# Performance work log

Hardware: AMD Instinct MI355X
Metric: run time of the kernel (lower is better)

The kernel has to match this reference:

```python
import jax, jax.numpy as jnp
import numpy as np

B, S, D, H, E, K = 2, 2048, 1024, 4096, 8, 2


def setup_inputs() -> dict:
    key = jax.random.key(0)
    ks = jax.random.split(key, 7)
    sd = 1.0 / np.sqrt(D)
    sh = 1.0 / np.sqrt(H)
    return {
        "x": jax.random.normal(ks[0], (B, S, D), dtype=jnp.float32),
        "Wr": jax.random.uniform(ks[1], (D, E), jnp.float32, -sd, sd),
        "br": jnp.zeros((E,), jnp.float32),
        "W1": jax.random.uniform(ks[2], (E, D, H), jnp.float32, -sd, sd),
        "b1": jax.random.uniform(ks[3], (E, H), jnp.float32, -sd, sd),
        "W2": jax.random.uniform(ks[4], (E, H, D), jnp.float32, -sh, sh),
        "b2": jax.random.uniform(ks[5], (E, D), jnp.float32, -sh, sh),
    }


def reference(x, Wr, br, W1, b1, W2, b2):
    # Router
    router_logits = jnp.einsum("bsd,de->bse", x, Wr) + br          # [B,S,E]
    topk_logits, topk_idx = jax.lax.top_k(router_logits, K)          # [B,S,K]
    gates = jax.nn.softmax(topk_logits, axis=-1)                     # [B,S,K]

    # Dense all-expert FFN (math identical to masked per-expert GEMMs)
    h = jax.nn.gelu(jnp.einsum("bsd,edh->ebsh", x, W1) + b1[:, None, None, :],
                    approximate=False)                                # [E,B,S,H]
    y = jnp.einsum("ebsh,ehd->bsed", h, W2) + b2[None, None, :, :]    # [B,S,E,D]

    # Gather the top-k experts per token and combine with gates
    sel = jnp.take_along_axis(y, topk_idx[..., None], axis=2)         # [B,S,K,D]
    out = jnp.sum(gates[..., None] * sel, axis=2)                     # [B,S,D]

    # Load-balancing aux loss
    probs = jax.nn.softmax(router_logits, axis=-1)
    importance = probs.mean(axis=(0, 1))                              # [E]
    aux_loss = jnp.mean((importance - 1.0 / E) ** 2)
    return out, aux_loss
```

## Files before the change

### kernel.cpp

```cpp
#include <hip/hip_runtime.h>
#include <hip/hip_bf16.h>
#include <math.h>

#define NTOK 4096
#define DD   1024
#define HH   4096
#define EE   8
#define NSLOT 8192
#define NSLOT_PAD 8320
#define RBLK 128

typedef __bf16 bf16x8 __attribute__((ext_vector_type(8)));
typedef float  f32x4  __attribute__((ext_vector_type(4)));
typedef unsigned short u16x8 __attribute__((ext_vector_type(8)));

#define WAITCNT_VM(n) (((n) & 0xF) | (0x7 << 4) | (0xF << 8) | (((n) >> 4) << 14))

#define WS_COUNTS     0
#define WS_CURSORS    64
#define WS_OFFSETS    128
#define WS_IMP        256
#define WS_TOPK_IDX   512
#define WS_TOPK_GATE  33280
#define WS_SLOT_OF    66048
#define WS_TOKEN_LIST 98816
#define WS_XG         131584
#define WS_HBUF       17170944
#define WS_YBUF       85328384
#define WS_W1BT       118882816
#define WS_W2BT       185991680
#define WS_CNT_PART   (WS_HBUF + (size_t)NSLOT * HH * 2)
#define WS_IMP_PART   (WS_HBUF + (size_t)NSLOT * HH * 2 + 4096)

__device__ __forceinline__ float gelu_exact(float v) {
    return 0.5f * v * (1.0f + erff(v * 0.70710678118654752f));
}

__device__ __forceinline__ void async_copy16(const __bf16* g, __bf16* l) {
    __builtin_amdgcn_global_load_lds(
        (const __attribute__((address_space(1))) void*)g,
        (__attribute__((address_space(3))) void*)l, 16, 0, 0);
}

__launch_bounds__(256)
__global__ void router_kernel(const float* __restrict__ x,
                              const float* __restrict__ Wr,
                              const float* __restrict__ br,
                              int* __restrict__ cntPart,
                              float* __restrict__ impPart,
                              int* __restrict__ topk_idx,
                              float* __restrict__ topk_gate) {
    __shared__ float WrL[DD * EE];
    __shared__ float impW[4][EE];
    __shared__ int cntL[EE];
    int tid = threadIdx.x;
    int lane = tid & 63, wave = tid >> 6;
    int grp = lane >> 3, e = lane & 7;
    int t = blockIdx.x * 32 + wave * 8 + grp;

    for (int i = tid; i < DD * EE / 4; i += 256)
        ((float4*)WrL)[i] = ((const float4*)Wr)[i];
    if (tid < EE) cntL[tid] = 0;
    __syncthreads();

    const float* xr = x + (size_t)t * DD;
    float acc = 0.f;
#pragma unroll 4
    for (int d = 0; d < DD; d += 4) {
        float4 xv = *(const float4*)(xr + d);
        acc = fmaf(xv.x, WrL[(d + 0) * EE + e], acc);
        acc = fmaf(xv.y, WrL[(d + 1) * EE + e], acc);
        acc = fmaf(xv.z, WrL[(d + 2) * EE + e], acc);
        acc = fmaf(xv.w, WrL[(d + 3) * EE + e], acc);
    }
    float l = acc + br[e];

    float m = l;
#pragma unroll
    for (int mk = 1; mk <= 4; mk <<= 1) m = fmaxf(m, __shfl_xor(m, mk, 64));
    float p = expf(l - m);
    float s = p;
#pragma unroll
    for (int mk = 1; mk <= 4; mk <<= 1) s += __shfl_xor(s, mk, 64);
    p /= s;

    float bl = l; int be = e;
#pragma unroll
    for (int mk = 1; mk <= 4; mk <<= 1) {
        float ol = __shfl_xor(bl, mk, 64);
        int   oe = __shfl_xor(be, mk, 64);
        if (ol > bl || (ol == bl && oe < be)) { bl = ol; be = oe; }
    }
    int e1 = be; float l1 = bl;
    float cl = (e == e1) ? -INFINITY : l; int ce = e;
#pragma unroll
    for (int mk = 1; mk <= 4; mk <<= 1) {
        float ol = __shfl_xor(cl, mk, 64);
        int   oe = __shfl_xor(ce, mk, 64);
        if (ol > cl || (ol == cl && oe < ce)) { cl = ol; ce = oe; }
    }
    int e2 = ce; float l2 = cl;

    if (e == 0) {
        float bb = expf(l2 - l1);
        float g1 = 1.f / (1.f + bb);
        topk_idx[t * 2 + 0] = e1; topk_idx[t * 2 + 1] = e2;
        topk_gate[t * 2 + 0] = g1; topk_gate[t * 2 + 1] = bb * g1;
        atomicAdd(&cntL[e1], 1);
        atomicAdd(&cntL[e2], 1);
    }

#pragma unroll
    for (int mk = 8; mk <= 32; mk <<= 1) p += __shfl_xor(p, mk, 64);
    if (lane < 8) impW[wave][lane] = p;
    __syncthreads();
    if (tid < EE) {
        float v = impW[0][tid] + impW[1][tid] + impW[2][tid] + impW[3][tid];
        impPart[blockIdx.x * EE + tid] = v;
        cntPart[blockIdx.x * EE + tid] = cntL[tid];
    }
}

__launch_bounds__(64)
__global__ void prefix_kernel(const int* __restrict__ cntPart,
                              const float* __restrict__ impPart,
                              int* __restrict__ offsets,
                              int* __restrict__ cursors,
                              float* __restrict__ aux_out) {
    __shared__ int cs[EE];
    __shared__ float is[EE];
    int tid = threadIdx.x;
    if (tid < EE) {
        int c = 0; float v = 0.f;
        for (int b = 0; b < RBLK; b++) {
            c += cntPart[b * EE + tid];
            v += impPart[b * EE + tid];
        }
        cs[tid] = c; is[tid] = v;
    }
    __syncthreads();
    if (tid == 0) {
        int o = 0;
        for (int e = 0; e < EE; e++) { offsets[e] = o; cursors[e] = o; o += cs[e]; }
        offsets[EE] = o;
        float aux = 0.f;
        for (int e = 0; e < EE; e++) {
            float d = is[e] / (float)NTOK - 1.0f / (float)EE;
            aux += d * d;
        }
        aux_out[0] = aux / (float)EE;
    }
}

__launch_bounds__(256)
__global__ void scatter_kernel(const int* __restrict__ topk_idx,
                               int* __restrict__ cursors,
                               int* __restrict__ token_list,
                               int* __restrict__ slot_of) {
    __shared__ int lcnt[EE];
    __shared__ int lbase[EE];
    int tid = threadIdx.x;
    int t = blockIdx.x * 256 + tid;
    if (tid < EE) lcnt[tid] = 0;
    __syncthreads();
    int e0 = topk_idx[t * 2 + 0], e1 = topk_idx[t * 2 + 1];
    int r0 = atomicAdd(&lcnt[e0], 1);
    int r1 = atomicAdd(&lcnt[e1], 1);
    __syncthreads();
    if (tid < EE) lbase[tid] = atomicAdd(&cursors[tid], lcnt[tid]);
    __syncthreads();
    int s0 = lbase[e0] + r0, s1 = lbase[e1] + r1;
    token_list[s0] = t; token_list[s1] = t;
    slot_of[t * 2 + 0] = s0; slot_of[t * 2 + 1] = s1;
}

__launch_bounds__(256)
__global__ void gather_x_kernel(const float* __restrict__ x,
                                const int* __restrict__ token_list,
                                __bf16* __restrict__ xg) {
    int s = blockIdx.x;
    int t = token_list[s];
    int tid = threadIdx.x;
    float4 v = ((const float4*)(x + (size_t)t * DD))[tid];
    __bf16 tmp[4] __attribute__((aligned(8)));
    tmp[0] = (__bf16)v.x; tmp[1] = (__bf16)v.y;
    tmp[2] = (__bf16)v.z; tmp[3] = (__bf16)v.w;
    ((ushort4*)(xg + (size_t)s * DD))[tid] = *(ushort4*)tmp;
}

__launch_bounds__(256)
__global__ void transpose_w_kernel(const float* __restrict__ in,
                                   __bf16* __restrict__ out,
                                   int R, int C) {
    int e = blockIdx.z;
    int c0 = blockIdx.x * 64, r0 = blockIdx.y * 64;
    __shared__ float tile[64][65];
    int tid = threadIdx.x;
    const float* ip = in + (size_t)e * R * C;
#pragma unroll
    for (int i = 0; i < 4; i++) {
        int flat = i * 256 + tid;
        int r = flat >> 4, c4 = (flat & 15) * 4;
        float4 v = *(const float4*)(ip + (size_t)(r0 + r) * C + c0 + c4);
        tile[r][c4 + 0] = v.x; tile[r][c4 + 1] = v.y;
        tile[r][c4 + 2] = v.z; tile[r][c4 + 3] = v.w;
    }
    __syncthreads();
    __bf16* op = out + (size_t)e * C * R;
#pragma unroll
    for (int i = 0; i < 2; i++) {
        int flat = i * 256 + tid;
        int c = flat >> 3, r8 = (flat & 7) * 8;
        __bf16 tmp[8] __attribute__((aligned(16)));
#pragma unroll
        for (int j = 0; j < 8; j++) tmp[j] = (__bf16)tile[r8 + j][c];
        *(u16x8*)(op + (size_t)(c0 + c) * R + r0 + r8) = *(u16x8*)tmp;
    }
}

template <int N, int K, bool GELU, typename OutT>
__launch_bounds__(256, 2)
__global__ void gemm_bt_kernel(const __bf16* __restrict__ A,
                               const __bf16* __restrict__ Bt,
                               const float* __restrict__ bias,
                               const int* __restrict__ offsets,
                               OutT* __restrict__ Out) {
    int e = blockIdx.z, ct = blockIdx.x, rt = blockIdx.y;
    int obase = offsets[e], cnt = offsets[e + 1] - obase;
    int m0 = rt * 128;
    if (m0 >= cnt) return;

    __shared__ __bf16 As[2][128 * 64];
    __shared__ __bf16 Bs[2][128 * 64];

    int tid = threadIdx.x, lane = tid & 63, wave = tid >> 6;
    int quad = lane >> 4, m16 = lane & 15;
    int wm = wave & 1, wn = wave >> 1;
    int srow = lane >> 3;
    int scol = ((lane & 7) ^ srow) * 8;
    int swz = m16 & 7;

    const __bf16* Ag = A + (size_t)(obase + m0) * K;
    const __bf16* Bg = Bt + ((size_t)e * N + (size_t)ct * 128) * K;

    f32x4 acc[4][4] = {};

#define STAGE(buf, k0)                                                        \
    {                                                                         \
        _Pragma("unroll")                                                     \
        for (int r = 0; r < 4; r++) {                                         \
            int chunk = r * 4 + wave;                       \
            int row = chunk * 8 + srow;                                       \
            async_copy16(Ag + (size_t)row * K + (k0) + scol, As[buf] + chunk * 512); \
        }                                                                     \
        _Pragma("unroll")                                                     \
        for (int r = 0; r < 4; r++) {                                         \
            int chunk = r * 4 + wave;                                         \
            int row = chunk * 8 + srow;                                       \
            async_copy16(Bg + (size_t)row * K + (k0) + scol, Bs[buf] + chunk * 512); \
        }                                                                     \
    }

#define COMPUTE(buf)                                                          \
    {                                                                         \
        const __bf16* Ac = As[buf];                                           \
        const __bf16* Bc = Bs[buf];                                           \
        _Pragma("unroll")                                                     \
        for (int kk = 0; kk < 64; kk += 32) {                                 \
            int kkc = kk >> 3;                                                \
            bf16x8 af[4], bfr[4];                                             \
            _Pragma("unroll")                                                 \
            for (int mi = 0; mi < 4; mi++)                                    \
                af[mi] = *(const bf16x8*)(Ac + (wm * 64 + mi * 16 + m16) * 64 \
                                          + (((kkc + quad) ^ swz) * 8));      \
            _Pragma("unroll")                                                 \
            for (int ni = 0; ni < 4; ni++)                                    \
                bfr[ni] = *(const bf16x8*)(Bc + (wn * 64 + ni * 16 + m16) * 64\
                                           + (((kkc + quad) ^ swz) * 8));     \
            _Pragma("unroll")                                                 \
            for (int mi = 0; mi < 4; mi++)                                    \
                _Pragma("unroll")                                             \
                for (int ni = 0; ni < 4; ni++)                                \
                    acc[mi][ni] = __builtin_amdgcn_mfma_f32_16x16x32_bf16(    \
                        af[mi], bfr[ni], acc[mi][ni], 0, 0, 0);               \
        }                                                                     \
    }

    STAGE(0, 0);
    int cur = 0;
    for (int k0 = 64; k0 < K; k0 += 64) {
        STAGE(cur ^ 1, k0);
        __builtin_amdgcn_s_waitcnt(WAITCNT_VM(8));
        __builtin_amdgcn_s_barrier();
        COMPUTE(cur);
        __builtin_amdgcn_s_barrier();
        cur ^= 1;
    }
    __builtin_amdgcn_s_waitcnt(WAITCNT_VM(0));
    __builtin_amdgcn_s_barrier();
    COMPUTE(cur);
#undef STAGE
#undef COMPUTE

    float bv[4];
#pragma unroll
    for (int ni = 0; ni < 4; ni++)
        bv[ni] = bias[(size_t)e * N + ct * 128 + wn * 64 + ni * 16 + m16];
#pragma unroll
    for (int mi = 0; mi < 4; mi++) {
#pragma unroll
        for (int r = 0; r < 4; r++) {
            int row = wm * 64 + mi * 16 + quad * 4 + r;
            if (m0 + row < cnt) {
                size_t orow = (size_t)(obase + m0 + row) * N + (size_t)ct * 128 + wn * 64;
#pragma unroll
                for (int ni = 0; ni < 4; ni++) {
                    float v = acc[mi][ni][r] + bv[ni];
                    if (GELU) v = gelu_exact(v);
                    Out[orow + ni * 16 + m16] = (OutT)v;
                }
            }
        }
    }
}

__launch_bounds__(256)
__global__ void combine_kernel(const float* __restrict__ ybuf,
                               const int* __restrict__ slot_of,
                               const float* __restrict__ topk_gate,
                               float* __restrict__ out) {
    int t = blockIdx.x;
    int tid = threadIdx.x;
    int s0 = slot_of[t * 2 + 0], s1 = slot_of[t * 2 + 1];
    float g0 = topk_gate[t * 2 + 0], g1 = topk_gate[t * 2 + 1];
    const float4* y0 = (const float4*)(ybuf + (size_t)s0 * DD);
    const float4* y1 = (const float4*)(ybuf + (size_t)s1 * DD);
    float4 a = y0[tid], b = y1[tid];
    float4 o;
    o.x = g0 * a.x + g1 * b.x;
    o.y = g0 * a.y + g1 * b.y;
    o.z = g0 * a.z + g1 * b.z;
    o.w = g0 * a.w + g1 * b.w;
    ((float4*)(out + (size_t)t * DD))[tid] = o;
}

extern "C" void kernel_launch(void* const* d_in, const int* in_sizes, int n_in,
                              void* d_out, int out_size, void* d_ws, size_t ws_size,
                              hipStream_t stream) {
    const float* x  = (const float*)d_in[0];
    const float* Wr = (const float*)d_in[1];
    const float* br = (const float*)d_in[2];
    const float* W1 = (const float*)d_in[3];
    const float* b1 = (const float*)d_in[4];
    const float* W2 = (const float*)d_in[5];
    const float* b2 = (const float*)d_in[6];
    float* out = (float*)d_out;

    char* ws = (char*)d_ws;
    int*    offsets    = (int*)(ws + WS_OFFSETS);
    int*    cursors    = (int*)(ws + WS_CURSORS);
    int*    topk_idx   = (int*)(ws + WS_TOPK_IDX);
    float*  topk_gate  = (float*)(ws + WS_TOPK_GATE);
    int*    slot_of    = (int*)(ws + WS_SLOT_OF);
    int*    token_list = (int*)(ws + WS_TOKEN_LIST);
    __bf16* xg         = (__bf16*)(ws + WS_XG);
    __bf16* hbuf       = (__bf16*)(ws + WS_HBUF);
    float*  ybuf       = (float*)(ws + WS_YBUF);
    __bf16* W1bt       = (__bf16*)(ws + WS_W1BT);
    __bf16* W2bt       = (__bf16*)(ws + WS_W2BT);
    int*    cntPart    = (int*)(ws + WS_CNT_PART);
    float*  impPart    = (float*)(ws + WS_IMP_PART);

    router_kernel<<<RBLK, 256, 0, stream>>>(x, Wr, br, cntPart, impPart, topk_idx, topk_gate);
    prefix_kernel<<<1, 64, 0, stream>>>(cntPart, impPart, offsets, cursors, out + (size_t)NTOK * DD);
    scatter_kernel<<<NTOK / 256, 256, 0, stream>>>(topk_idx, cursors, token_list, slot_of);
    gather_x_kernel<<<NSLOT, 256, 0, stream>>>(x, token_list, xg);

    transpose_w_kernel<<<dim3(HH / 64, DD / 64, EE), 256, 0, stream>>>(W1, W1bt, DD, HH);
    transpose_w_kernel<<<dim3(DD / 64, HH / 64, EE), 256, 0, stream>>>(W2, W2bt, HH, DD);

    gemm_bt_kernel<HH, DD, true, __bf16>
        <<<dim3(HH / 128, NSLOT / 128, EE), 256, 0, stream>>>(xg, W1bt, b1, offsets, hbuf);
    gemm_bt_kernel<DD, HH, false, float>
        <<<dim3(DD / 128, NSLOT / 128, EE), 256, 0, stream>>>(hbuf, W2bt, b2, offsets, ybuf);

    combine_kernel<<<NTOK, 256, 0, stream>>>(ybuf, slot_of, topk_gate, out);
}
```

Before: 655.9 us.

## Replace grouped GEMM with 8-wave 256-row tiles and interleaved half-tile pipelining

Replaces the 128x128, 4-wave grouped expert GEMM with an 8-wave, 512-thread kernel that uses 256-row tiles and 256- or 128-column tiles. Each 64-wide K step is split into half-tile stages that interleave LDS reads, async global-to-LDS copies and MFMA groups, and MFMA sections are wrapped in s_setprio. The larger tiles raise arithmetic intensity and cut redundant global loads, while the finer interleaving aims to hide load latency behind compute. The cost is more register and LDS pressure, padding waste when expert row counts are not multiples of 256, and workspace offsets shifted to fit a larger pad.

```diff
diff --git a/kernel.cpp b/kernel.cpp
--- a/kernel.cpp
+++ b/kernel.cpp
@@ -7,7 +7,7 @@
 #define HH   4096
 #define EE   8
 #define NSLOT 8192
-#define NSLOT_PAD 8320
+#define NSLOT_PAD 8448
 #define RBLK 128
 
 typedef __bf16 bf16x8 __attribute__((ext_vector_type(8)));
@@ -25,10 +25,10 @@
 #define WS_SLOT_OF    66048
 #define WS_TOKEN_LIST 98816
 #define WS_XG         131584
-#define WS_HBUF       17170944
-#define WS_YBUF       85328384
-#define WS_W1BT       118882816
-#define WS_W2BT       185991680
+#define WS_HBUF       17433088
+#define WS_YBUF       86639104
+#define WS_W1BT       120193536
+#define WS_W2BT       187302400
 #define WS_CNT_PART   (WS_HBUF + (size_t)NSLOT * HH * 2)
 #define WS_IMP_PART   (WS_HBUF + (size_t)NSLOT * HH * 2 + 4096)
 
@@ -218,106 +218,178 @@
     }
 }
 
-template <int N, int K, bool GELU, typename OutT>
-__launch_bounds__(256, 2)
-__global__ void gemm_bt_kernel(const __bf16* __restrict__ A,
-                               const __bf16* __restrict__ Bt,
-                               const float* __restrict__ bias,
-                               const int* __restrict__ offsets,
-                               OutT* __restrict__ Out) {
+template <int N, int K, int BN, bool GELU, typename OutT>
+__launch_bounds__(512, 2)
+__global__ void gemm8p_kernel(const __bf16* __restrict__ A,
+                              const __bf16* __restrict__ Bt,
+                              const float* __restrict__ bias,
+                              const int* __restrict__ offsets,
+                              OutT* __restrict__ Out) {
+    constexpr int BM  = 256;
+    constexpr int NHB = BN / 128;
+    constexpr int WGN = (BN == 256) ? 4 : 2;
+    constexpr int WGM = 8 / WGN;
+    constexpr int MF  = BM / (WGM * 16);
+    constexpr int NF  = BN / (WGN * 16);
+    constexpr int APF = MF / 2;
+    constexpr int BPF = (NHB == 2) ? 2 : NF;
+    constexpr int NT  = K / 64;
+
     int e = blockIdx.z, ct = blockIdx.x, rt = blockIdx.y;
     int obase = offsets[e], cnt = offsets[e + 1] - obase;
-    int m0 = rt * 128;
+    int m0 = rt * BM;
     if (m0 >= cnt) return;
 
-    __shared__ __bf16 As[2][128 * 64];
-    __shared__ __bf16 Bs[2][128 * 64];
+    __shared__ __bf16 As[2][2][16 * 512];
+    __shared__ __bf16 Bs[2][NHB][16 * 512];
 
     int tid = threadIdx.x, lane = tid & 63, wave = tid >> 6;
     int quad = lane >> 4, m16 = lane & 15;
-    int wm = wave & 1, wn = wave >> 1;
+    int wm = wave & (WGM - 1), wn = wave / WGM;
     int srow = lane >> 3;
     int scol = ((lane & 7) ^ srow) * 8;
-    int swz = m16 & 7;
-
-    const __bf16* Ag = A + (size_t)(obase + m0) * K;
-    const __bf16* Bg = Bt + ((size_t)e * N + (size_t)ct * 128) * K;
-
-    f32x4 acc[4][4] = {};
-
-#define STAGE(buf, k0)                                                        \
-    {                                                                         \
-        _Pragma("unroll")                                                     \
-        for (int r = 0; r < 4; r++) {                                         \
-            int chunk = r * 4 + wave;                       \
-            int row = chunk * 8 + srow;                                       \
-            async_copy16(Ag + (size_t)row * K + (k0) + scol, As[buf] + chunk * 512); \
-        }                                                                     \
-        _Pragma("unroll")                                                     \
-        for (int r = 0; r < 4; r++) {                                         \
-            int chunk = r * 4 + wave;                                         \
-            int row = chunk * 8 + srow;                                       \
-            async_copy16(Bg + (size_t)row * K + (k0) + scol, Bs[buf] + chunk * 512); \
-        }                                                                     \
-    }
-
-#define COMPUTE(buf)                                                          \
-    {                                                                         \
-        const __bf16* Ac = As[buf];                                           \
-        const __bf16* Bc = Bs[buf];                                           \
-        _Pragma("unroll")                                                     \
-        for (int kk = 0; kk < 64; kk += 32) {                                 \
-            int kkc = kk >> 3;                                                \
-            bf16x8 af[4], bfr[4];                                             \
-            _Pragma("unroll")                                                 \
-            for (int mi = 0; mi < 4; mi++)                                    \
-                af[mi] = *(const bf16x8*)(Ac + (wm * 64 + mi * 16 + m16) * 64 \
-                                          + (((kkc + quad) ^ swz) * 8));      \
-            _Pragma("unroll")                                                 \
-            for (int ni = 0; ni < 4; ni++)                                    \
-                bfr[ni] = *(const bf16x8*)(Bc + (wn * 64 + ni * 16 + m16) * 64\
-                                           + (((kkc + quad) ^ swz) * 8));     \
-            _Pragma("unroll")                                                 \
-            for (int mi = 0; mi < 4; mi++)                                    \
-                _Pragma("unroll")                                             \
-                for (int ni = 0; ni < 4; ni++)                                \
-                    acc[mi][ni] = __builtin_amdgcn_mfma_f32_16x16x32_bf16(    \
-                        af[mi], bfr[ni], acc[mi][ni], 0, 0, 0);               \
-        }                                                                     \
-    }
-
-    STAGE(0, 0);
+
+    const __bf16* Ag = A + (size_t)(obase + m0) * K + scol;
+    const __bf16* Bg = Bt + ((size_t)e * N + (size_t)ct * BN) * K + scol;
+
+    const __bf16* pA[2][2];
+    const __bf16* pB[NHB][2];
+#pragma unroll
+    for (int h = 0; h < 2; h++)
+#pragma unroll
+        for (int r = 0; r < 2; r++)
+            pA[h][r] = Ag + (size_t)(h * 128 + r * 64 + wave * 8 + srow) * K;
+#pragma unroll
+    for (int h = 0; h < NHB; h++)
+#pragma unroll
+        for (int r = 0; r < 2; r++)
+            pB[h][r] = Bg + (size_t)(h * 128 + r * 64 + wave * 8 + srow) * K;
+
+    f32x4 acc[MF][NF] = {};
+    bf16x8 af[APF][2], bfr[NF][2];
+
+#define STG_A(buf, h, k0)                                                     \
+    { async_copy16(pA[h][0] + (k0), &As[buf][h][wave * 512]);                 \
+      async_copy16(pA[h][1] + (k0), &As[buf][h][(wave + 8) * 512]); }
+#define STG_B(buf, h, k0)                                                     \
+    { async_copy16(pB[h][0] + (k0), &Bs[buf][h][wave * 512]);                 \
+      async_copy16(pB[h][1] + (k0), &Bs[buf][h][(wave + 8) * 512]); }
+
+#define READ_A(buf, mh)                                                       \
+    { _Pragma("unroll")                                                       \
+      for (int mi = 0; mi < APF; mi++) {                                      \
+          int r = (mi * WGM + wm) * 16 + m16;                                 \
+          const __bf16* bp = &As[buf][mh][(r >> 3) * 512 + (r & 7) * 64];     \
+          af[mi][0] = *(const bf16x8*)(bp + ((quad ^ (r & 7)) * 8));          \
+          af[mi][1] = *(const bf16x8*)(bp + (((4 + quad) ^ (r & 7)) * 8)); } }
+#define READ_B(buf, nh, nn)                                                   \
+    { _Pragma("unroll")                                                       \
+      for (int ni = 0; ni < (nn); ni++) {                                     \
+          int r = (ni * WGN + wn) * 16 + m16;                                 \
+          const __bf16* bp = &Bs[buf][nh][(r >> 3) * 512 + (r & 7) * 64];     \
+          bfr[(nh) * 2 + ni][0] = *(const bf16x8*)(bp + ((quad ^ (r & 7)) * 8)); \
+          bfr[(nh) * 2 + ni][1] = *(const bf16x8*)(bp + (((4 + quad) ^ (r & 7)) * 8)); } }
+
+#define MMA(mh, nh)                                                           \
+    { __builtin_amdgcn_s_setprio(1);                                         \
+      _Pragma("unroll")                                                       \
+      for (int kk = 0; kk < 2; kk++)                                          \
+          _Pragma("unroll")                                                   \
+          for (int mi = 0; mi < APF; mi++)                                    \
+              _Pragma("unroll")                                               \
+              for (int ni = 0; ni < BPF; ni++)                                \
+                  acc[(mh) * APF + mi][(nh) * 2 + ni] =                       \
+                      __builtin_amdgcn_mfma_f32_16x16x32_bf16(                \
+                          af[mi][kk], bfr[(nh) * 2 + ni][kk],                 \
+                          acc[(mh) * APF + mi][(nh) * 2 + ni], 0, 0, 0);      \
+      __builtin_amdgcn_s_setprio(0); }
+
+    STG_A(0, 0, 0);
+    STG_B(0, 0, 0);
+    if constexpr (NHB == 2) STG_B(0, 1, 0);
+    STG_A(0, 1, 0);
+
     int cur = 0;
-    for (int k0 = 64; k0 < K; k0 += 64) {
-        STAGE(cur ^ 1, k0);
-        __builtin_amdgcn_s_waitcnt(WAITCNT_VM(8));
+    for (int t = 0; t < NT - 1; t++) {
+        int k1 = (t + 1) * 64;
+        int nxt = cur ^ 1;
+        if constexpr (NHB == 2) {
+            __builtin_amdgcn_s_waitcnt(WAITCNT_VM(4));
+            __builtin_amdgcn_s_barrier();
+            READ_A(cur, 0); READ_B(cur, 0, 2);
+            STG_A(nxt, 0, k1); STG_B(nxt, 0, k1);
+            MMA(0, 0);
+            __builtin_amdgcn_s_waitcnt(WAITCNT_VM(6));
+            __builtin_amdgcn_s_barrier();
+            READ_B(cur, 1, 2);
+            STG_B(nxt, 1, k1);
+            MMA(0, 1);
+            __builtin_amdgcn_s_waitcnt(WAITCNT_VM(6));
+            __builtin_amdgcn_s_barrier();
+            READ_A(cur, 1);
+            STG_A(nxt, 1, k1);
+            MMA(1, 1);
+            MMA(1, 0);
+        } else {
+            __builtin_amdgcn_s_waitcnt(WAITCNT_VM(2));
+            __builtin_amdgcn_s_barrier();
+            READ_A(cur, 0); READ_B(cur, 0, 4);
+            STG_A(nxt, 0, k1); STG_B(nxt, 0, k1);
+            MMA(0, 0);
+            __builtin_amdgcn_s_waitcnt(WAITCNT_VM(4));
+            __builtin_amdgcn_s_barrier();
+            READ_A(cur, 1);
+            STG_A(nxt, 1, k1);
+            MMA(1, 0);
+        }
+        cur = nxt;
+    }
+    if constexpr (NHB == 2) {
+        __builtin_amdgcn_s_waitcnt(WAITCNT_VM(4));
         __builtin_amdgcn_s_barrier();
-        COMPUTE(cur);
+        READ_A(cur, 0); READ_B(cur, 0, 2);
+        MMA(0, 0);
+        __builtin_amdgcn_s_waitcnt(WAITCNT_VM(2));
         __builtin_amdgcn_s_barrier();
-        cur ^= 1;
-    }
-    __builtin_amdgcn_s_waitcnt(WAITCNT_VM(0));
-    __builtin_amdgcn_s_barrier();
-    COMPUTE(cur);
-#undef STAGE
-#undef COMPUTE
-
-    float bv[4];
-#pragma unroll
-    for (int ni = 0; ni < 4; ni++)
-        bv[ni] = bias[(size_t)e * N + ct * 128 + wn * 64 + ni * 16 + m16];
-#pragma unroll
-    for (int mi = 0; mi < 4; mi++) {
-#pragma unroll
-        for (int r = 0; r < 4; r++) {
-            int row = wm * 64 + mi * 16 + quad * 4 + r;
+        READ_B(cur, 1, 2);
+        MMA(0, 1);
+        __builtin_amdgcn_s_waitcnt(WAITCNT_VM(0));
+        __builtin_amdgcn_s_barrier();
+        READ_A(cur, 1);
+        MMA(1, 1);
+        MMA(1, 0);
+    } else {
+        __builtin_amdgcn_s_waitcnt(WAITCNT_VM(2));
+        __builtin_amdgcn_s_barrier();
+        READ_A(cur, 0); READ_B(cur, 0, 4);
+        MMA(0, 0);
+        __builtin_amdgcn_s_waitcnt(WAITCNT_VM(0));
+        __builtin_amdgcn_s_barrier();
+        READ_A(cur, 1);
+        MMA(1, 0);
+    }
+#undef STG_A
+#undef STG_B
+#undef READ_A
+#undef READ_B
+#undef MMA
+
+    float bv[NF];
+#pragma unroll
+    for (int ni = 0; ni < NF; ni++)
+        bv[ni] = bias[(size_t)e * N + ct * BN + (ni * WGN + wn) * 16 + m16];
+#pragma unroll
+    for (int mi = 0; mi < MF; mi++) {
+#pragma unroll
+        for (int rr = 0; rr < 4; rr++) {
+            int row = (mi * WGM + wm) * 16 + quad * 4 + rr;
             if (m0 + row < cnt) {
-                size_t orow = (size_t)(obase + m0 + row) * N + (size_t)ct * 128 + wn * 64;
-#pragma unroll
-                for (int ni = 0; ni < 4; ni++) {
-                    float v = acc[mi][ni][r] + bv[ni];
+                size_t orow = (size_t)(obase + m0 + row) * N + (size_t)ct * BN;
+#pragma unroll
+                for (int ni = 0; ni < NF; ni++) {
+                    float v = acc[mi][ni][rr] + bv[ni];
                     if (GELU) v = gelu_exact(v);
-                    Out[orow + ni * 16 + m16] = (OutT)v;
+                    Out[orow + (ni * WGN + wn) * 16 + m16] = (OutT)v;
                 }
             }
         }
@@ -379,10 +451,10 @@
     transpose_w_kernel<<<dim3(HH / 64, DD / 64, EE), 256, 0, stream>>>(W1, W1bt, DD, HH);
     transpose_w_kernel<<<dim3(DD / 64, HH / 64, EE), 256, 0, stream>>>(W2, W2bt, HH, DD);
 
-    gemm_bt_kernel<HH, DD, true, __bf16>
-        <<<dim3(HH / 128, NSLOT / 128, EE), 256, 0, stream>>>(xg, W1bt, b1, offsets, hbuf);
-    gemm_bt_kernel<DD, HH, false, float>
-        <<<dim3(DD / 128, NSLOT / 128, EE), 256, 0, stream>>>(hbuf, W2bt, b2, offsets, ybuf);
+    gemm8p_kernel<HH, DD, 256, true, __bf16>
+        <<<dim3(HH / 256, 16, EE), 512, 0, stream>>>(xg, W1bt, b1, offsets, hbuf);
+    gemm8p_kernel<DD, HH, 128, false, float>
+        <<<dim3(DD / 128, 16, EE), 512, 0, stream>>>(hbuf, W2bt, b2, offsets, ybuf);
 
     combine_kernel<<<NTOK, 256, 0, stream>>>(ybuf, slot_of, topk_gate, out);
 }
```

Result: faster. 632.9 us (-3.5%).

## Rewrite grouped MoE GEMM with 8-wave blocks and split-phase A/B pipelining

Applied to the files above, without the earlier changes.

The grouped GEMM moves from 4 waves of 64x64 tiles to 8 waves, each computing a 32x64 sub-tile. Each K step is split into two half-phases with separate A buffers, so async global-to-LDS loads for the next step interleave with MFMA work, and s_setprio raises MFMA priority. The row-tile grid shrinks from 64 to 32 per expert, on the assumption that no expert gets more than 4096 slots. The workspace padding changes to match. The aim is better latency hiding and occupancy, at the cost of finer barriers and a fixed cap on tokens per expert.

```diff
diff --git a/kernel.cpp b/kernel.cpp
--- a/kernel.cpp
+++ b/kernel.cpp
@@ -7,7 +7,7 @@
 #define HH   4096
 #define EE   8
 #define NSLOT 8192
-#define NSLOT_PAD 8320
+#define NSLOT_PAD 8448
 #define RBLK 128
 
 typedef __bf16 bf16x8 __attribute__((ext_vector_type(8)));
@@ -25,10 +25,10 @@
 #define WS_SLOT_OF    66048
 #define WS_TOKEN_LIST 98816
 #define WS_XG         131584
-#define WS_HBUF       17170944
-#define WS_YBUF       85328384
-#define WS_W1BT       118882816
-#define WS_W2BT       185991680
+#define WS_HBUF       17433088
+#define WS_YBUF       86639104
+#define WS_W1BT       120193536
+#define WS_W2BT       187302400
 #define WS_CNT_PART   (WS_HBUF + (size_t)NSLOT * HH * 2)
 #define WS_IMP_PART   (WS_HBUF + (size_t)NSLOT * HH * 2 + 4096)
 
@@ -219,105 +219,120 @@
 }
 
 template <int N, int K, bool GELU, typename OutT>
-__launch_bounds__(256, 2)
-__global__ void gemm_bt_kernel(const __bf16* __restrict__ A,
+__launch_bounds__(512, 4)
+__global__ void gemm128_kernel(const __bf16* __restrict__ A,
                                const __bf16* __restrict__ Bt,
                                const float* __restrict__ bias,
                                const int* __restrict__ offsets,
                                OutT* __restrict__ Out) {
+    constexpr int NT = K / 64;
     int e = blockIdx.z, ct = blockIdx.x, rt = blockIdx.y;
     int obase = offsets[e], cnt = offsets[e + 1] - obase;
     int m0 = rt * 128;
     if (m0 >= cnt) return;
 
-    __shared__ __bf16 As[2][128 * 64];
-    __shared__ __bf16 Bs[2][128 * 64];
+    __shared__ __bf16 As[2][2][8 * 512];
+    __shared__ __bf16 Bs[2][16 * 512];
 
     int tid = threadIdx.x, lane = tid & 63, wave = tid >> 6;
     int quad = lane >> 4, m16 = lane & 15;
-    int wm = wave & 1, wn = wave >> 1;
+    int wm = wave & 3, wn = wave >> 2;
     int srow = lane >> 3;
     int scol = ((lane & 7) ^ srow) * 8;
+
+    const __bf16* Ag = A + (size_t)(obase + m0) * K + scol;
+    const __bf16* Bg = Bt + ((size_t)e * N + (size_t)ct * 128) * K + scol;
+
+    const __bf16* pA[2];
+    const __bf16* pB[2];
+#pragma unroll
+    for (int h = 0; h < 2; h++) pA[h] = Ag + (size_t)(h * 64 + wave * 8 + srow) * K;
+#pragma unroll
+    for (int p = 0; p < 2; p++) pB[p] = Bg + (size_t)(p * 64 + wave * 8 + srow) * K;
+
     int swz = m16 & 7;
-
-    const __bf16* Ag = A + (size_t)(obase + m0) * K;
-    const __bf16* Bg = Bt + ((size_t)e * N + (size_t)ct * 128) * K;
-
-    f32x4 acc[4][4] = {};
-
-#define STAGE(buf, k0)                                                        \
-    {                                                                         \
-        _Pragma("unroll")                                                     \
-        for (int r = 0; r < 4; r++) {                                         \
-            int chunk = r * 4 + wave;                       \
-            int row = chunk * 8 + srow;                                       \
-            async_copy16(Ag + (size_t)row * K + (k0) + scol, As[buf] + chunk * 512); \
-        }                                                                     \
-        _Pragma("unroll")                                                     \
-        for (int r = 0; r < 4; r++) {                                         \
-            int chunk = r * 4 + wave;                                         \
-            int row = chunk * 8 + srow;                                       \
-            async_copy16(Bg + (size_t)row * K + (k0) + scol, Bs[buf] + chunk * 512); \
-        }                                                                     \
-    }
-
-#define COMPUTE(buf)                                                          \
-    {                                                                         \
-        const __bf16* Ac = As[buf];                                           \
-        const __bf16* Bc = Bs[buf];                                           \
-        _Pragma("unroll")                                                     \
-        for (int kk = 0; kk < 64; kk += 32) {                                 \
-            int kkc = kk >> 3;                                                \
-            bf16x8 af[4], bfr[4];                                             \
-            _Pragma("unroll")                                                 \
-            for (int mi = 0; mi < 4; mi++)                                    \
-                af[mi] = *(const bf16x8*)(Ac + (wm * 64 + mi * 16 + m16) * 64 \
-                                          + (((kkc + quad) ^ swz) * 8));      \
-            _Pragma("unroll")                                                 \
-            for (int ni = 0; ni < 4; ni++)                                    \
-                bfr[ni] = *(const bf16x8*)(Bc + (wn * 64 + ni * 16 + m16) * 64\
-                                           + (((kkc + quad) ^ swz) * 8));     \
-            _Pragma("unroll")                                                 \
-            for (int mi = 0; mi < 4; mi++)                                    \
-                _Pragma("unroll")                                             \
-                for (int ni = 0; ni < 4; ni++)                                \
-                    acc[mi][ni] = __builtin_amdgcn_mfma_f32_16x16x32_bf16(    \
-                        af[mi], bfr[ni], acc[mi][ni], 0, 0, 0);               \
-        }                                                                     \
-    }
-
-    STAGE(0, 0);
+    int abase = (wm * 2 + (m16 >> 3)) * 512 + swz * 64;
+    int bbase[4];
+#pragma unroll
+    for (int ni = 0; ni < 4; ni++)
+        bbase[ni] = (ni * 4 + wn * 2 + (m16 >> 3)) * 512 + swz * 64;
+
+    f32x4 acc[2][4] = {};
+    bf16x8 af[2], bfr[4][2];
+
+#define STG_A(buf, h, k0) async_copy16(pA[h] + (k0), &As[buf][h][wave * 512]);
+#define STG_B(buf, k0)                                                        \
+    { async_copy16(pB[0] + (k0), &Bs[buf][wave * 512]);                       \
+      async_copy16(pB[1] + (k0), &Bs[buf][(wave + 8) * 512]); }
+
+#define READ_A(buf, h)                                                        \
+    { af[0] = *(const bf16x8*)(&As[buf][h][abase] + ((quad ^ swz) * 8));      \
+      af[1] = *(const bf16x8*)(&As[buf][h][abase] + (((4 + quad) ^ swz) * 8)); }
+#define READ_B(buf)                                                           \
+    { _Pragma("unroll")                                                       \
+      for (int ni = 0; ni < 4; ni++) {                                        \
+          bfr[ni][0] = *(const bf16x8*)(&Bs[buf][bbase[ni]] + ((quad ^ swz) * 8)); \
+          bfr[ni][1] = *(const bf16x8*)(&Bs[buf][bbase[ni]] + (((4 + quad) ^ swz) * 8)); } }
+
+#define MMA(h)                                                                \
+    { __builtin_amdgcn_s_setprio(1);                                         \
+      _Pragma("unroll")                                                       \
+      for (int kk = 0; kk < 2; kk++)                                          \
+          _Pragma("unroll")                                                   \
+          for (int ni = 0; ni < 4; ni++)                                      \
+              acc[h][ni] = __builtin_amdgcn_mfma_f32_16x16x32_bf16(           \
+                  af[kk], bfr[ni][kk], acc[h][ni], 0, 0, 0);                  \
+      __builtin_amdgcn_s_setprio(0); }
+
+    STG_A(0, 0, 0);
+    STG_B(0, 0);
+    STG_A(0, 1, 0);
+
     int cur = 0;
-    for (int k0 = 64; k0 < K; k0 += 64) {
-        STAGE(cur ^ 1, k0);
-        __builtin_amdgcn_s_waitcnt(WAITCNT_VM(8));
+    for (int t = 0; t < NT - 1; t++) {
+        int k1 = (t + 1) * 64, nxt = cur ^ 1;
+        __builtin_amdgcn_s_waitcnt(WAITCNT_VM(1));
         __builtin_amdgcn_s_barrier();
-        COMPUTE(cur);
+        READ_A(cur, 0); READ_B(cur);
+        STG_A(nxt, 0, k1); STG_B(nxt, k1);
+        MMA(0);
+        __builtin_amdgcn_s_waitcnt(WAITCNT_VM(3));
         __builtin_amdgcn_s_barrier();
-        cur ^= 1;
-    }
+        READ_A(cur, 1);
+        STG_A(nxt, 1, k1);
+        MMA(1);
+        cur = nxt;
+    }
+    __builtin_amdgcn_s_waitcnt(WAITCNT_VM(1));
+    __builtin_amdgcn_s_barrier();
+    READ_A(cur, 0); READ_B(cur);
+    MMA(0);
     __builtin_amdgcn_s_waitcnt(WAITCNT_VM(0));
     __builtin_amdgcn_s_barrier();
-    COMPUTE(cur);
-#undef STAGE
-#undef COMPUTE
+    READ_A(cur, 1);
+    MMA(1);
+#undef STG_A
+#undef STG_B
+#undef READ_A
+#undef READ_B
+#undef MMA
 
     float bv[4];
 #pragma unroll
     for (int ni = 0; ni < 4; ni++)
-        bv[ni] = bias[(size_t)e * N + ct * 128 + wn * 64 + ni * 16 + m16];
-#pragma unroll
-    for (int mi = 0; mi < 4; mi++) {
-#pragma unroll
-        for (int r = 0; r < 4; r++) {
-            int row = wm * 64 + mi * 16 + quad * 4 + r;
+        bv[ni] = bias[(size_t)e * N + ct * 128 + (ni * 2 + wn) * 16 + m16];
+#pragma unroll
+    for (int mi = 0; mi < 2; mi++) {
+#pragma unroll
+        for (int rr = 0; rr < 4; rr++) {
+            int row = (mi * 4 + wm) * 16 + quad * 4 + rr;
             if (m0 + row < cnt) {
-                size_t orow = (size_t)(obase + m0 + row) * N + (size_t)ct * 128 + wn * 64;
+                size_t orow = (size_t)(obase + m0 + row) * N + (size_t)ct * 128;
 #pragma unroll
                 for (int ni = 0; ni < 4; ni++) {
-                    float v = acc[mi][ni][r] + bv[ni];
+                    float v = acc[mi][ni][rr] + bv[ni];
                     if (GELU) v = gelu_exact(v);
-                    Out[orow + ni * 16 + m16] = (OutT)v;
+                    Out[orow + (ni * 2 + wn) * 16 + m16] = (OutT)v;
                 }
             }
         }
@@ -379,10 +394,10 @@
     transpose_w_kernel<<<dim3(HH / 64, DD / 64, EE), 256, 0, stream>>>(W1, W1bt, DD, HH);
     transpose_w_kernel<<<dim3(DD / 64, HH / 64, EE), 256, 0, stream>>>(W2, W2bt, HH, DD);
 
-    gemm_bt_kernel<HH, DD, true, __bf16>
-        <<<dim3(HH / 128, NSLOT / 128, EE), 256, 0, stream>>>(xg, W1bt, b1, offsets, hbuf);
-    gemm_bt_kernel<DD, HH, false, float>
-        <<<dim3(DD / 128, NSLOT / 128, EE), 256, 0, stream>>>(hbuf, W2bt, b2, offsets, ybuf);
+    gemm128_kernel<HH, DD, true, __bf16>
+        <<<dim3(HH / 128, 32, EE), 512, 0, stream>>>(xg, W1bt, b1, offsets, hbuf);
+    gemm128_kernel<DD, HH, false, float>
+        <<<dim3(DD / 128, 32, EE), 512, 0, stream>>>(hbuf, W2bt, b2, offsets, ybuf);
 
     combine_kernel<<<NTOK, 256, 0, stream>>>(ybuf, slot_of, topk_gate, out);
 }
```

Result: faster. 622.4 us (-5.1%).
